# Optimization experiments

Hardware: AMD Instinct MI355X
Metric: run time of the kernel (lower is better)

## Reference

```python
import jax, jax.numpy as jnp
import numpy as np

NODE_IN = 128
NODE_OUT = 128
LEAKY_SLOPE = 0.01  # torch nn.LeakyReLU default


def setup_inputs() -> dict:
    key = jax.random.key(0)
    k1, k2, k3, k4 = jax.random.split(key, 4)
    B, N = 64, 1024
    node_mat = jax.random.normal(k1, (B, N, NODE_IN), dtype=jnp.float32)
    adj_mat = jax.random.uniform(k2, (B, N, N), dtype=jnp.float32)
    # Linear(node_in_len, node_out_len): W [out, in], b [out] (torch default init style)
    bound = 1.0 / np.sqrt(NODE_IN)
    W = jax.random.uniform(k3, (NODE_OUT, NODE_IN), minval=-bound, maxval=bound, dtype=jnp.float32)
    b = jax.random.uniform(k4, (NODE_OUT,), minval=-bound, maxval=bound, dtype=jnp.float32)
    return {"node_mat": node_mat, "adj_mat": adj_mat, "W": W, "b": b}


def reference(node_mat, adj_mat, W, b):
    # n_neighbors[b,i] = sum_j adj[b,i,j]; diag(1/deg) @ adj == adj / deg (row-wise)
    deg = jnp.sum(adj_mat, axis=-1, keepdims=True)          # [B,N,1]
    norm_adj = adj_mat / deg                                 # [B,N,N]
    agg = jnp.einsum('bij,bjf->bif', norm_adj, node_mat)     # [B,N,Fin]
    out = jnp.einsum('bif,of->bio', agg, W) + b              # [B,N,Fout]
    return jnp.where(out >= 0, out, LEAKY_SLOPE * out)
```

## Files before the change

kernel.cpp:

```cpp
#include <hip/hip_runtime.h>
#include <hip/hip_bf16.h>


typedef __attribute__((ext_vector_type(8))) short bf16x8;
typedef __attribute__((ext_vector_type(4))) float f32x4;

__device__ __forceinline__ unsigned f2bf(float x) {
  unsigned u = __builtin_bit_cast(unsigned, x);
  u += 0x7FFFu + ((u >> 16) & 1u);
  return u >> 16;
}
__device__ __forceinline__ int f2bf2(float x, float y) {
  return (int)(f2bf(x) | (f2bf(y) << 16));
}

__device__ __forceinline__ void gload_lds16(const void* g, void* l) {
  __builtin_amdgcn_global_load_lds(
      (const __attribute__((address_space(1))) unsigned int*)g,
      (__attribute__((address_space(3))) unsigned int*)l, 16, 0, 0);
}

#define JPAD 136

__global__ __launch_bounds__(256) void k_ht(const float* __restrict__ node,
                                            const float* __restrict__ W,
                                            ushort* __restrict__ Ht) {
  __shared__ short nt[128 * JPAD];
  __shared__ short wt[128 * JPAD];
  const int b = blockIdx.y, jt = blockIdx.x, t = threadIdx.x;
  const float4* nbase = (const float4*)(node + (size_t)(b * 1024 + jt * 128) * 128);
  const float4* wbase = (const float4*)W;

  #pragma unroll
  for (int p = 0; p < 16; p++) {
    int idx = t + 256 * p;
    int r = idx >> 5, c4 = idx & 31;
    float4 v = nbase[idx];
    int2 s; s.x = f2bf2(v.x, v.y); s.y = f2bf2(v.z, v.w);
    *(int2*)&nt[r * JPAD + c4 * 4] = s;
    float4 wv = wbase[idx];
    int2 sw; sw.x = f2bf2(wv.x, wv.y); sw.y = f2bf2(wv.z, wv.w);
    *(int2*)&wt[r * JPAD + c4 * 4] = sw;
  }
  __syncthreads();

  const int lane = t & 63, wid = t >> 6;
  const int q = lane >> 4, r = lane & 15;
  const int wm = wid & 1, wn = wid >> 1;
  f32x4 acc[4][4] = {};
  #pragma unroll
  for (int ks = 0; ks < 4; ks++) {
    bf16x8 af[4], bg[4];
    #pragma unroll
    for (int mi = 0; mi < 4; mi++)
      af[mi] = *(const bf16x8*)&nt[(wm * 64 + mi * 16 + r) * JPAD + ks * 32 + q * 8];
    #pragma unroll
    for (int ni = 0; ni < 4; ni++)
      bg[ni] = *(const bf16x8*)&wt[(wn * 64 + ni * 16 + r) * JPAD + ks * 32 + q * 8];
    #pragma unroll
    for (int mi = 0; mi < 4; mi++)
      #pragma unroll
      for (int ni = 0; ni < 4; ni++)
        acc[mi][ni] = __builtin_amdgcn_mfma_f32_16x16x32_bf16(af[mi], bg[ni], acc[mi][ni], 0, 0, 0);
  }
  __syncthreads();

  #pragma unroll
  for (int mi = 0; mi < 4; mi++)
    #pragma unroll
    for (int ni = 0; ni < 4; ni++)
      #pragma unroll
      for (int v = 0; v < 4; v++) {
        int j = wm * 64 + mi * 16 + q * 4 + v;
        int o = wn * 64 + ni * 16 + r;
        nt[o * JPAD + j] = (short)f2bf(acc[mi][ni][v]);
      }
  __syncthreads();
  {
    int o = t >> 1, half = t & 1;
    const int4* src = (const int4*)&nt[o * JPAD + half * 64];
    int4* dst = (int4*)(Ht + (size_t)b * 131072 + (size_t)o * 1024 + jt * 128 + half * 64);
    #pragma unroll
    for (int i = 0; i < 8; i++) dst[i] = src[i];
  }
}

__global__ __launch_bounds__(256) void k_main(const float* __restrict__ adj,
                                              const ushort* __restrict__ Ht,
                                              const float* __restrict__ bias,
                                              float* __restrict__ out) {
  __shared__ short hbuf[2][128 * 64];
  const int b = blockIdx.y, it = blockIdx.x, t = threadIdx.x;
  const int lane = t & 63, wid = t >> 6;
  const int q = lane >> 4, r = lane & 15;
  const int i0 = it * 64 + wid * 16;
  const float4* ap = (const float4*)(adj + (size_t)(b * 1024 + i0 + r) * 1024);

  const int o_l = wid * 32 + (lane >> 3);
  const int cchunk = (lane & 7) ^ ((lane >> 3) & 7);
  const ushort* gsrc = Ht + (size_t)b * 131072 + (size_t)o_l * 1024 + cchunk * 8;

  const int boff0 = r * 128 + (((0 * 4 + q) ^ (r & 7)) << 4);
  const int boff1 = r * 128 + (((1 * 4 + q) ^ (r & 7)) << 4);

  f32x4 acc[8] = {};
  float rs = 0.f;

  #pragma unroll
  for (int p = 0; p < 4; p++)
    gload_lds16(gsrc + (size_t)p * 8192, &hbuf[0][(wid * 32 + 8 * p) * 64]);
  float4 a0 = ap[q * 2], a1 = ap[q * 2 + 1], a2 = ap[q * 2 + 8], a3 = ap[q * 2 + 9];
  __syncthreads();

  int c = 0;
  #pragma unroll 1
  for (int kt = 0; kt < 16; kt++) {
    if (kt < 15) {
      #pragma unroll
      for (int p = 0; p < 4; p++)
        gload_lds16(gsrc + (size_t)p * 8192 + (kt + 1) * 64,
                    &hbuf[c ^ 1][(wid * 32 + 8 * p) * 64]);
    }

    union { bf16x8 v; int i[4]; } u0, u1;
    u0.i[0] = f2bf2(a0.x, a0.y); u0.i[1] = f2bf2(a0.z, a0.w);
    u0.i[2] = f2bf2(a1.x, a1.y); u0.i[3] = f2bf2(a1.z, a1.w);
    u1.i[0] = f2bf2(a2.x, a2.y); u1.i[1] = f2bf2(a2.z, a2.w);
    u1.i[2] = f2bf2(a3.x, a3.y); u1.i[3] = f2bf2(a3.z, a3.w);
    rs += (a0.x + a0.y + a0.z + a0.w) + (a1.x + a1.y + a1.z + a1.w)
        + (a2.x + a2.y + a2.z + a2.w) + (a3.x + a3.y + a3.z + a3.w);

    const int nb = (kt < 15 ? kt + 1 : 15) * 16 + q * 2;
    float4 n0 = ap[nb], n1 = ap[nb + 1], n2 = ap[nb + 8], n3 = ap[nb + 9];

    const char* hb = (const char*)&hbuf[c][0];
    int4 bv[8];
    #pragma unroll
    for (int ni = 0; ni < 8; ni++) bv[ni] = *(const int4*)(hb + boff0 + ni * 2048);
    #pragma unroll
    for (int ni = 0; ni < 8; ni++)
      acc[ni] = __builtin_amdgcn_mfma_f32_16x16x32_bf16(
          u0.v, __builtin_bit_cast(bf16x8, bv[ni]), acc[ni], 0, 0, 0);
    #pragma unroll
    for (int ni = 0; ni < 8; ni++) bv[ni] = *(const int4*)(hb + boff1 + ni * 2048);
    #pragma unroll
    for (int ni = 0; ni < 8; ni++)
      acc[ni] = __builtin_amdgcn_mfma_f32_16x16x32_bf16(
          u1.v, __builtin_bit_cast(bf16x8, bv[ni]), acc[ni], 0, 0, 0);

    a0 = n0; a1 = n1; a2 = n2; a3 = n3;
    __syncthreads();
    c ^= 1;
  }

  rs += __shfl_xor(rs, 16);
  rs += __shfl_xor(rs, 32);

  float* obase = out + (size_t)(b * 1024 + i0) * 128;
  #pragma unroll
  for (int v = 0; v < 4; v++) {
    const float rd = 1.0f / __shfl(rs, q * 4 + v);
    const int i = q * 4 + v;
    #pragma unroll
    for (int ni = 0; ni < 8; ni++) {
      float val = acc[ni][v] * rd + bias[ni * 16 + r];
      val = val >= 0.0f ? val : 0.01f * val;
      obase[(size_t)i * 128 + ni * 16 + r] = val;
    }
  }
}

__global__ __launch_bounds__(256) void k_fallback(const float* __restrict__ node,
                                                  const float* __restrict__ adj,
                                                  const float* __restrict__ W,
                                                  const float* __restrict__ bias,
                                                  float* __restrict__ out) {
  __shared__ float red[256];
  __shared__ float agg[128];
  const int b = blockIdx.y, i = blockIdx.x, t = threadIdx.x;
  const float* arow = adj + (size_t)(b * 1024 + i) * 1024;
  float s = 0.f;
  for (int j = t; j < 1024; j += 256) s += arow[j];
  red[t] = s;
  __syncthreads();
  if (t < 128) red[t] += red[t + 128];
  __syncthreads();
  if (t < 64) {
    float v2 = red[t] + red[t + 64];
    #pragma unroll
    for (int off = 32; off; off >>= 1) v2 += __shfl_down(v2, off);
    if (t == 0) red[0] = v2;
  }
  __syncthreads();
  const float rdeg = 1.0f / red[0];
  const int f = t & 127, half = t >> 7;
  const float* nb = node + (size_t)b * 1024 * 128;
  float a = 0.f;
  for (int j = half * 512; j < half * 512 + 512; j++)
    a += arow[j] * nb[(size_t)j * 128 + f];
  __syncthreads();
  if (half == 0) agg[f] = a;
  __syncthreads();
  if (half == 1) agg[f] += a;
  __syncthreads();
  if (t < 128) {
    const float* wr = W + t * 128;
    float o = 0.f;
    for (int f2 = 0; f2 < 128; f2++) o += agg[f2] * wr[f2];
    o = o * rdeg + bias[t];
    out[(size_t)(b * 1024 + i) * 128 + t] = o >= 0.f ? o : 0.01f * o;
  }
}

extern "C" void kernel_launch(void* const* d_in, const int* in_sizes, int n_in,
                              void* d_out, int out_size, void* d_ws, size_t ws_size,
                              hipStream_t stream) {
  const float* node = (const float*)d_in[0];
  const float* adj  = (const float*)d_in[1];
  const float* W    = (const float*)d_in[2];
  const float* bias = (const float*)d_in[3];
  float* out = (float*)d_out;
  const size_t ht_bytes = (size_t)64 * 128 * 1024 * 2;
  if (ws_size >= ht_bytes) {
    ushort* Ht = (ushort*)d_ws;
    k_ht<<<dim3(8, 64), 256, 0, stream>>>(node, W, Ht);
    k_main<<<dim3(16, 64), 256, 0, stream>>>(adj, Ht, bias, out);
  } else {
    k_fallback<<<dim3(1024, 64), 256, 0, stream>>>(node, adj, W, bias, out);
  }
}
```

Baseline: 411.9 us.

## Triple-buffer k_main with prefetch distance two and partial vmcnt waits

Moves k_main from double to triple buffering. Both the LDS tiles of Ht and the register copies of the adjacency rows are now fetched two k-steps ahead. The full __syncthreads is replaced by `s_waitcnt vmcnt(8)` plus a raw barrier, so the loads for step kt+2 stay in flight while step kt+1's data is guaranteed ready. The loop is fully unrolled and launch bounds request 3 waves per SIMD, which keeps occupancy under the larger 48KB LDS footprint. The aim is to hide global-memory latency on the adj stream. The cost is more register pressure and a hand-counted waitcnt that depends on exactly 8 loads being issued per step.

Result: slower. 422.4 us (+2.5%).

```diff
diff --git a/kernel.cpp b/kernel.cpp
--- a/kernel.cpp
+++ b/kernel.cpp
@@ -85,11 +85,11 @@
   }
 }
 
-__global__ __launch_bounds__(256) void k_main(const float* __restrict__ adj,
-                                              const ushort* __restrict__ Ht,
-                                              const float* __restrict__ bias,
-                                              float* __restrict__ out) {
-  __shared__ short hbuf[2][128 * 64];
+__global__ __launch_bounds__(256, 3) void k_main(const float* __restrict__ adj,
+                                                 const ushort* __restrict__ Ht,
+                                                 const float* __restrict__ bias,
+                                                 float* __restrict__ out) {
+  __shared__ short hbuf[3][128 * 64];
   const int b = blockIdx.y, it = blockIdx.x, t = threadIdx.x;
   const int lane = t & 63, wid = t >> 6;
   const int q = lane >> 4, r = lane & 15;
@@ -105,24 +105,33 @@
 
   f32x4 acc[8] = {};
   float rs = 0.f;
+  float4 areg[3][4];
 
   #pragma unroll
   for (int p = 0; p < 4; p++)
     gload_lds16(gsrc + (size_t)p * 8192, &hbuf[0][(wid * 32 + 8 * p) * 64]);
-  float4 a0 = ap[q * 2], a1 = ap[q * 2 + 1], a2 = ap[q * 2 + 8], a3 = ap[q * 2 + 9];
-  __syncthreads();
-
-  int c = 0;
-  #pragma unroll 1
+  {
+    const int nb = q * 2;
+    areg[0][0] = ap[nb]; areg[0][1] = ap[nb + 1];
+    areg[0][2] = ap[nb + 8]; areg[0][3] = ap[nb + 9];
+  }
+  #pragma unroll
+  for (int p = 0; p < 4; p++)
+    gload_lds16(gsrc + (size_t)p * 8192 + 64, &hbuf[1][(wid * 32 + 8 * p) * 64]);
+  {
+    const int nb = 16 + q * 2;
+    areg[1][0] = ap[nb]; areg[1][1] = ap[nb + 1];
+    areg[1][2] = ap[nb + 8]; areg[1][3] = ap[nb + 9];
+  }
+  asm volatile("s_waitcnt vmcnt(8)" ::: "memory");
+  __builtin_amdgcn_s_barrier();
+
+  #pragma unroll
   for (int kt = 0; kt < 16; kt++) {
-    if (kt < 15) {
-      #pragma unroll
-      for (int p = 0; p < 4; p++)
-        gload_lds16(gsrc + (size_t)p * 8192 + (kt + 1) * 64,
-                    &hbuf[c ^ 1][(wid * 32 + 8 * p) * 64]);
-    }
-
+    const int cur = kt % 3, nx2 = (kt + 2) % 3;
+    const int ktn = (kt < 14) ? kt + 2 : 15;
     union { bf16x8 v; int i[4]; } u0, u1;
+    float4 a0 = areg[cur][0], a1 = areg[cur][1], a2 = areg[cur][2], a3 = areg[cur][3];
     u0.i[0] = f2bf2(a0.x, a0.y); u0.i[1] = f2bf2(a0.z, a0.w);
     u0.i[2] = f2bf2(a1.x, a1.y); u0.i[3] = f2bf2(a1.z, a1.w);
     u1.i[0] = f2bf2(a2.x, a2.y); u1.i[1] = f2bf2(a2.z, a2.w);
@@ -130,10 +139,16 @@
     rs += (a0.x + a0.y + a0.z + a0.w) + (a1.x + a1.y + a1.z + a1.w)
         + (a2.x + a2.y + a2.z + a2.w) + (a3.x + a3.y + a3.z + a3.w);
 
-    const int nb = (kt < 15 ? kt + 1 : 15) * 16 + q * 2;
-    float4 n0 = ap[nb], n1 = ap[nb + 1], n2 = ap[nb + 8], n3 = ap[nb + 9];
-
-    const char* hb = (const char*)&hbuf[c][0];
+    #pragma unroll
+    for (int p = 0; p < 4; p++)
+      gload_lds16(gsrc + (size_t)p * 8192 + ktn * 64, &hbuf[nx2][(wid * 32 + 8 * p) * 64]);
+    {
+      const int nb = ktn * 16 + q * 2;
+      areg[nx2][0] = ap[nb]; areg[nx2][1] = ap[nb + 1];
+      areg[nx2][2] = ap[nb + 8]; areg[nx2][3] = ap[nb + 9];
+    }
+
+    const char* hb = (const char*)&hbuf[cur][0];
     int4 bv[8];
     #pragma unroll
     for (int ni = 0; ni < 8; ni++) bv[ni] = *(const int4*)(hb + boff0 + ni * 2048);
@@ -148,9 +163,8 @@
       acc[ni] = __builtin_amdgcn_mfma_f32_16x16x32_bf16(
           u1.v, __builtin_bit_cast(bf16x8, bv[ni]), acc[ni], 0, 0, 0);
 
-    a0 = n0; a1 = n1; a2 = n2; a3 = n3;
-    __syncthreads();
-    c ^= 1;
+    asm volatile("s_waitcnt vmcnt(8)" ::: "memory");
+    __builtin_amdgcn_s_barrier();
   }
 
   rs += __shfl_xor(rs, 16);
```
